# Kernel tuning notes

Hardware: AMD Instinct MI355X
Metric: run time of the kernel (lower is better)

Reference implementation:

```python
import jax, jax.numpy as jnp
import numpy as np

D_MODEL = 1024
D_STATE = 16
EXPAND = 2
D_CONV = 4
D_INNER = EXPAND * D_MODEL          # 2048
DT_RANK = D_MODEL // 16             # 64
B = 2
L = 1024
EPS = 1e-5


def setup_inputs() -> dict:
    key = jax.random.key(0)
    ks = jax.random.split(key, 8)
    s = 0.02
    return {
        "x": jax.random.normal(ks[0], (B, L, D_MODEL), jnp.float32),
        "ln_gamma": jnp.ones((D_MODEL,), jnp.float32),
        "ln_beta": jnp.zeros((D_MODEL,), jnp.float32),
        "in_proj_w": jax.random.normal(ks[1], (2 * D_INNER, D_MODEL), jnp.float32) * s,
        "conv_w": jax.random.normal(ks[2], (D_INNER, 1, D_CONV), jnp.float32) * s,
        "conv_b": jnp.zeros((D_INNER,), jnp.float32),
        "x_proj_w": jax.random.normal(ks[3], (DT_RANK + 2 * D_STATE, D_INNER), jnp.float32) * s,
        "dt_proj_w": jax.random.normal(ks[4], (D_INNER, DT_RANK), jnp.float32) * s,
        "dt_proj_b": jax.random.normal(ks[5], (D_INNER,), jnp.float32) * 0.01,
        "A_log": jnp.log(jnp.tile(jnp.arange(1, D_STATE + 1, dtype=jnp.float32), (D_INNER, 1))),
        "D_skip": jnp.ones((D_INNER,), jnp.float32),
        "out_proj_w": jax.random.normal(ks[6], (D_MODEL, D_INNER), jnp.float32) * s,
    }


def _layernorm(x, g, b):
    mu = jnp.mean(x, axis=-1, keepdims=True)
    var = jnp.mean((x - mu) ** 2, axis=-1, keepdims=True)
    return (x - mu) * jax.lax.rsqrt(var + EPS) * g + b


def _mamba_forward(x, ln_gamma, ln_beta, in_proj_w, conv_w, conv_b,
                   x_proj_w, dt_proj_w, dt_proj_b, A_log, D_skip, out_proj_w):
    residual = x
    xn = _layernorm(x, ln_gamma, ln_beta)

    # in_proj -> split into ssm input u and gate z   (b, l, 2*d_inner)
    xz = jnp.einsum('bld,ed->ble', xn, in_proj_w)
    u, z = jnp.split(xz, 2, axis=-1)

    # causal depthwise conv1d (padding = d_conv-1 on the left, truncated to L)
    uc = jnp.transpose(u, (0, 2, 1))  # (b, d_inner, l)
    uc = jax.lax.conv_general_dilated(
        uc, conv_w, window_strides=(1,), padding=[(D_CONV - 1, 0)],
        feature_group_count=D_INNER,
        dimension_numbers=('NCH', 'OIH', 'NCH'))
    uc = uc + conv_b[None, :, None]
    u = jax.nn.silu(jnp.transpose(uc, (0, 2, 1)))  # (b, l, d_inner)

    # selective SSM
    A = -jnp.exp(A_log)                              # (d_inner, d_state)
    x_dbl = jnp.einsum('bld,ed->ble', u, x_proj_w)   # (b, l, dt_rank+2*n)
    dt, Bm, Cm = jnp.split(x_dbl, [DT_RANK, DT_RANK + D_STATE], axis=-1)
    delta = jax.nn.softplus(jnp.einsum('blr,dr->bld', dt, dt_proj_w) + dt_proj_b)

    def step(h, inputs):
        d_t, B_t, C_t, u_t = inputs            # (b,di) (b,n) (b,n) (b,di)
        dA = jnp.exp(d_t[..., None] * A)       # (b, di, n)
        h = dA * h + (d_t * u_t)[..., None] * B_t[:, None, :]
        y = jnp.einsum('bdn,bn->bd', h, C_t)
        return h, y

    h0 = jnp.zeros((x.shape[0], D_INNER, D_STATE), x.dtype)
    xs = (jnp.moveaxis(delta, 1, 0), jnp.moveaxis(Bm, 1, 0),
          jnp.moveaxis(Cm, 1, 0), jnp.moveaxis(u, 1, 0))
    _, ys = jax.lax.scan(step, h0, xs)
    y = jnp.moveaxis(ys, 0, 1) + u * D_skip     # (b, l, d_inner)

    y = y * jax.nn.silu(z)                      # gated output
    out = jnp.einsum('ble,de->bld', y, out_proj_w)
    # dropout is identity in eval mode
    return out + residual


def reference(x, ln_gamma, ln_beta, in_proj_w, conv_w, conv_b,
              x_proj_w, dt_proj_w, dt_proj_b, A_log, D_skip, out_proj_w):
    return _mamba_forward(x, ln_gamma, ln_beta, in_proj_w, conv_w, conv_b,
                          x_proj_w, dt_proj_w, dt_proj_b, A_log, D_skip, out_proj_w)
```

## Files before the change

### kernel.cpp

```cpp
#include <hip/hip_runtime.h>

#define D_MODEL 1024
#define D_STATE 16
#define D_INNER 2048
#define DT_RANK 64
#define NBATCH 2
#define SEQ_L 1024
#define M_ROWS (NBATCH * SEQ_L)
#define CHUNK 32
#define NCHUNK (SEQ_L / CHUNK)

typedef __bf16 bf16x8 __attribute__((ext_vector_type(8)));
typedef float f32x4 __attribute__((ext_vector_type(4)));
typedef unsigned short u16;
typedef unsigned int u32;
typedef u16 u16x4 __attribute__((ext_vector_type(4)));
typedef u16 u16x8 __attribute__((ext_vector_type(8)));

__device__ __forceinline__ float bf2f(u16 h) {
    return __uint_as_float(((unsigned)h) << 16);
}
__device__ __forceinline__ u16 f2bf(float f) {
    unsigned u = __float_as_uint(f);
    u += 0x7fff + ((u >> 16) & 1);
    return (u16)(u >> 16);
}

__global__ __launch_bounds__(256) void prep(
    const float* __restrict__ s0, const float* __restrict__ s1,
    const float* __restrict__ s2, const float* __restrict__ s3,
    u16* __restrict__ d0, u16* __restrict__ d1,
    u16* __restrict__ d2, u16* __restrict__ d3,
    const float* __restrict__ x, const float* __restrict__ g,
    const float* __restrict__ b, u16* __restrict__ xn,
    float* __restrict__ xd) {
    int blk = blockIdx.x;
    if (blk < 6464) {
        int idx = blk * 256 + threadIdx.x;
        const float4* s; u16* dp; int i;
        if (idx < 1048576)      { s = (const float4*)s0; i = idx;           dp = d0; }
        else if (idx < 1572864) { s = (const float4*)s1; i = idx - 1048576; dp = d1; }
        else if (idx < 1622016) { s = (const float4*)s2; i = idx - 1572864; dp = d2; }
        else                    { s = (const float4*)s3; i = idx - 1622016; dp = d3; }
        float4 v = s[i];
        u16x4 o = {f2bf(v.x), f2bf(v.y), f2bf(v.z), f2bf(v.w)};
        *(u16x4*)(dp + (size_t)i * 4) = o;
        return;
    }
    if (blk < 6656) {
        int zi = (blk - 6464) * 256 + threadIdx.x;
        ((float4*)xd)[zi] = (float4){0.f, 0.f, 0.f, 0.f};
        return;
    }
    int row = blk - 6656;
    const float4* xr = (const float4*)(x + (size_t)row * D_MODEL);
    float4 v = xr[threadIdx.x];
    float s  = v.x + v.y + v.z + v.w;
    float ss = v.x * v.x + v.y * v.y + v.z * v.z + v.w * v.w;
#pragma unroll
    for (int off = 32; off > 0; off >>= 1) {
        s  += __shfl_down(s,  off, 64);
        ss += __shfl_down(ss, off, 64);
    }
    __shared__ float sh_s[4], sh_ss[4];
    int wid = threadIdx.x >> 6;
    if ((threadIdx.x & 63) == 0) { sh_s[wid] = s; sh_ss[wid] = ss; }
    __syncthreads();
    float mu  = (sh_s[0] + sh_s[1] + sh_s[2] + sh_s[3]) * (1.0f / D_MODEL);
    float var = (sh_ss[0] + sh_ss[1] + sh_ss[2] + sh_ss[3]) * (1.0f / D_MODEL) - mu * mu;
    float rs = rsqrtf(var + 1e-5f);
    int c0 = threadIdx.x * 4;
    float vv[4] = {v.x, v.y, v.z, v.w};
#pragma unroll
    for (int j = 0; j < 4; j++) {
        int c = c0 + j;
        float o = (vv[j] - mu) * rs * g[c] + b[c];
        xn[(size_t)row * D_MODEL + c] = f2bf(o);
    }
}

template <int BM, int BN, int WM, int WN, int MODE>
__global__ __launch_bounds__(256) void gemm_lds(
    const __bf16* __restrict__ A, const __bf16* __restrict__ W,
    int K, int Ksteps, int ldC,
    float* __restrict__ outF, u16* __restrict__ outB) {
    constexpr int WCOLS = BN / (WN * 16);
    __shared__ __bf16 As[BM * 32];
    __shared__ __bf16 Bs[BN * 32];
    int tid  = threadIdx.x;
    int lane = tid & 63;
    int wid  = tid >> 6;
    int l16  = lane & 15;
    int quad = lane >> 4;
    int wr = wid / WCOLS;
    int wc = wid % WCOLS;
    int m0 = blockIdx.y * BM;
    int n0 = blockIdx.x * BN;
    int kbase = blockIdx.z * Ksteps * 32;

    f32x4 acc[WM][WN];
#pragma unroll
    for (int mi = 0; mi < WM; mi++)
#pragma unroll
        for (int nj = 0; nj < WN; nj++)
            acc[mi][nj] = (f32x4){0.f, 0.f, 0.f, 0.f};

    for (int ki = 0; ki < Ksteps; ki++) {
        int k0 = kbase + ki * 32;
        __syncthreads();
#pragma unroll
        for (int i = 0; i < BM / 64; i++) {
            int t   = i * 256 + tid;
            int row = t >> 2;
            int cg  = (t & 3) ^ ((row >> 1) & 3);
            __builtin_amdgcn_global_load_lds(
                (const __attribute__((address_space(1))) u32*)(A + (size_t)(m0 + row) * K + k0 + cg * 8),
                (__attribute__((address_space(3))) u32*)(As + (i * 256 + wid * 64) * 8),
                16, 0, 0);
        }
#pragma unroll
        for (int i = 0; i < BN / 64; i++) {
            int t   = i * 256 + tid;
            int row = t >> 2;
            int cg  = (t & 3) ^ ((row >> 1) & 3);
            __builtin_amdgcn_global_load_lds(
                (const __attribute__((address_space(1))) u32*)(W + (size_t)(n0 + row) * K + k0 + cg * 8),
                (__attribute__((address_space(3))) u32*)(Bs + (i * 256 + wid * 64) * 8),
                16, 0, 0);
        }
        __syncthreads();

        bf16x8 af[WM], bfr[WN];
#pragma unroll
        for (int mi = 0; mi < WM; mi++) {
            int r  = wr * WM * 16 + mi * 16 + l16;
            int cg = quad ^ ((r >> 1) & 3);
            af[mi] = *(const bf16x8*)(As + r * 32 + cg * 8);
        }
#pragma unroll
        for (int nj = 0; nj < WN; nj++) {
            int r  = wc * WN * 16 + nj * 16 + l16;
            int cg = quad ^ ((r >> 1) & 3);
            bfr[nj] = *(const bf16x8*)(Bs + r * 32 + cg * 8);
        }
#pragma unroll
        for (int mi = 0; mi < WM; mi++)
#pragma unroll
            for (int nj = 0; nj < WN; nj++)
                acc[mi][nj] = __builtin_amdgcn_mfma_f32_16x16x32_bf16(
                    af[mi], bfr[nj], acc[mi][nj], 0, 0, 0);
    }

    float* outP = (MODE == 4) ? outF + (size_t)blockIdx.z * M_ROWS * ldC : outF;
#pragma unroll
    for (int mi = 0; mi < WM; mi++) {
#pragma unroll
        for (int nj = 0; nj < WN; nj++) {
            int col = n0 + wc * WN * 16 + nj * 16 + l16;
#pragma unroll
            for (int r = 0; r < 4; r++) {
                int row = m0 + wr * WM * 16 + mi * 16 + quad * 4 + r;
                float v = acc[mi][nj][r];
                if (MODE == 0) {
                    outB[(size_t)row * ldC + col] = f2bf(v);
                } else {
                    outP[(size_t)row * ldC + col] = v;
                }
            }
        }
    }
}

__global__ __launch_bounds__(256) void out_reduce(
    const float* __restrict__ p, const float* __restrict__ x,
    float* __restrict__ out) {
    int idx = blockIdx.x * 256 + threadIdx.x;
    const int N = M_ROWS * D_MODEL;
    float4 a = ((const float4*)p)[idx];
    float4 b = ((const float4*)(p + N))[idx];
    float4 c = ((const float4*)(p + 2 * N))[idx];
    float4 d = ((const float4*)(p + 3 * N))[idx];
    float4 r = ((const float4*)x)[idx];
    float4 o;
    o.x = a.x + b.x + c.x + d.x + r.x;
    o.y = a.y + b.y + c.y + d.y + r.y;
    o.z = a.z + b.z + c.z + d.z + r.z;
    o.w = a.w + b.w + c.w + d.w + r.w;
    ((float4*)out)[idx] = o;
}

__global__ __launch_bounds__(256) void gemm_xp(
    const __bf16* __restrict__ A, const __bf16* __restrict__ W,
    float* __restrict__ outF) {
    const int K = D_INNER, Ksplit = D_INNER / 8, Nw = 96;
    int lane = threadIdx.x & 63;
    int wid  = threadIdx.x >> 6;
    int m0 = blockIdx.y * 64;
    int n0 = blockIdx.x * 64;
    int kc = blockIdx.z;
    int l16  = lane & 15;
    int quad = lane >> 4;
    int mrow = m0 + wid * 16 + l16;

    const __bf16* ap = A + (size_t)mrow * K + kc * Ksplit + quad * 8;
    const __bf16* wp[4];
#pragma unroll
    for (int j = 0; j < 4; j++) {
        int nc = n0 + j * 16 + l16;
        if (nc > Nw - 1) nc = Nw - 1;
        wp[j] = W + (size_t)nc * K + kc * Ksplit + quad * 8;
    }
    f32x4 acc[4];
#pragma unroll
    for (int j = 0; j < 4; j++) acc[j] = (f32x4){0.f, 0.f, 0.f, 0.f};

    for (int k = 0; k < Ksplit; k += 32) {
        bf16x8 a = *(const bf16x8*)ap;
        ap += 32;
#pragma unroll
        for (int j = 0; j < 4; j++) {
            bf16x8 bfr = *(const bf16x8*)wp[j];
            wp[j] += 32;
            acc[j] = __builtin_amdgcn_mfma_f32_16x16x32_bf16(a, bfr, acc[j], 0, 0, 0);
        }
    }
#pragma unroll
    for (int j = 0; j < 4; j++) {
        int col = n0 + j * 16 + l16;
        if (col < Nw) {
#pragma unroll
            for (int r = 0; r < 4; r++) {
                int row = m0 + wid * 16 + quad * 4 + r;
                atomicAdd(outF + (size_t)row * 96 + col, acc[j][r]);
            }
        }
    }
}

__global__ __launch_bounds__(256) void gemm_dt(
    const float* __restrict__ A, const __bf16* __restrict__ W,
    const float* __restrict__ bias, u16* __restrict__ outB16) {
    int lane = threadIdx.x & 63;
    int wid  = threadIdx.x >> 6;
    int m0 = blockIdx.y * 64;
    int n0 = blockIdx.x * 64;
    int l16  = lane & 15;
    int quad = lane >> 4;
    int mrow = m0 + wid * 16 + l16;

    const float* ap = A + (size_t)mrow * 96 + quad * 8;
    const __bf16* wp[4];
#pragma unroll
    for (int j = 0; j < 4; j++) {
        int nc = n0 + j * 16 + l16;
        wp[j] = W + (size_t)nc * DT_RANK + quad * 8;
    }
    f32x4 acc[4];
#pragma unroll
    for (int j = 0; j < 4; j++) acc[j] = (f32x4){0.f, 0.f, 0.f, 0.f};

#pragma unroll
    for (int k = 0; k < DT_RANK; k += 32) {
        float4 v0 = *(const float4*)(ap);
        float4 v1 = *(const float4*)(ap + 4);
        ap += 32;
        u16x8 pk;
        pk[0] = f2bf(v0.x); pk[1] = f2bf(v0.y); pk[2] = f2bf(v0.z); pk[3] = f2bf(v0.w);
        pk[4] = f2bf(v1.x); pk[5] = f2bf(v1.y); pk[6] = f2bf(v1.z); pk[7] = f2bf(v1.w);
        bf16x8 a = __builtin_bit_cast(bf16x8, pk);
#pragma unroll
        for (int j = 0; j < 4; j++) {
            bf16x8 bfr = *(const bf16x8*)wp[j];
            wp[j] += 32;
            acc[j] = __builtin_amdgcn_mfma_f32_16x16x32_bf16(a, bfr, acc[j], 0, 0, 0);
        }
    }
#pragma unroll
    for (int j = 0; j < 4; j++) {
        int col = n0 + j * 16 + l16;
#pragma unroll
        for (int r = 0; r < 4; r++) {
            int row = m0 + wid * 16 + quad * 4 + r;
            float t = acc[j][r] + bias[col];
            float sp = (t > 20.f) ? t : log1pf(__expf(t));
            outB16[(size_t)row * D_INNER + col] = f2bf(sp);
        }
    }
}

__global__ __launch_bounds__(256) void conv_silu(
    const u16* __restrict__ xz, const float* __restrict__ cw,
    const float* __restrict__ cb, u16* __restrict__ uc) {
    int idx = blockIdx.x * 256 + threadIdx.x;
    int base = idx * 8;
    int d = base & (D_INNER - 1);
    int m = base >> 11;
    int t = m & (SEQ_L - 1);
    float s[8];
    {
        float4 b0 = *(const float4*)(cb + d);
        float4 b1 = *(const float4*)(cb + d + 4);
        s[0] = b0.x; s[1] = b0.y; s[2] = b0.z; s[3] = b0.w;
        s[4] = b1.x; s[5] = b1.y; s[6] = b1.z; s[7] = b1.w;
    }
#pragma unroll
    for (int j = 0; j < 4; j++) {
        int tt = t - 3 + j;
        if (tt >= 0) {
            u16x8 uv = *(const u16x8*)(xz + (size_t)(m - 3 + j) * (2 * D_INNER) + d);
#pragma unroll
            for (int q = 0; q < 8; q++) {
                s[q] += cw[(d + q) * 4 + j] * bf2f(uv[q]);
            }
        }
    }
    u16x8 o;
#pragma unroll
    for (int q = 0; q < 8; q++) {
        float sig = 1.f / (1.f + __expf(-s[q]));
        o[q] = f2bf(s[q] * sig);
    }
    *(u16x8*)(uc + base) = o;
}

__global__ __launch_bounds__(256) void scan_chunk(
    const u16* __restrict__ delta, const u16* __restrict__ uc,
    const float* __restrict__ xd, const float* __restrict__ A_log,
    float* __restrict__ Pst, float* __restrict__ Sst) {
    __shared__ float Bsh[CHUNK][16];
    int tid  = threadIdx.x;
    int lane = tid & 63;
    int w    = tid >> 6;
    int dsub = lane & 15;
    int g    = lane >> 4;
    int n0   = g * 4;
    int c = blockIdx.x, b = blockIdx.z;
    int d = blockIdx.y * 64 + w * 16 + dsub;
    int mbase = b * SEQ_L + c * CHUNK;

    if (tid < CHUNK * 4) {
        int row = tid >> 2, q = tid & 3;
        *(float4*)&Bsh[row][q * 4] =
            *(const float4*)(xd + (size_t)(mbase + row) * 96 + DT_RANK + q * 4);
    }
    __syncthreads();

    float a[4];
    {
        float4 a0 = *(const float4*)(A_log + d * D_STATE + n0);
        a[0] = -__expf(a0.x); a[1] = -__expf(a0.y);
        a[2] = -__expf(a0.z); a[3] = -__expf(a0.w);
    }
    float P[4] = {1.f, 1.f, 1.f, 1.f}, S[4] = {0.f, 0.f, 0.f, 0.f};

    for (int t0 = 0; t0 < CHUNK; t0 += 4) {
        float dlv[4], uv[4];
#pragma unroll
        for (int i = 0; i < 4; i++) {
            int m = mbase + t0 + i;
            dlv[i] = bf2f(delta[(size_t)m * D_INNER + d]);
            uv[i]  = bf2f(uc[(size_t)m * D_INNER + d]);
        }
#pragma unroll
        for (int i = 0; i < 4; i++) {
            float c1 = dlv[i] * uv[i];
#pragma unroll
            for (int j = 0; j < 4; j++) {
                float dA = __expf(dlv[i] * a[j]);
                P[j] *= dA;
                S[j] = dA * S[j] + c1 * Bsh[t0 + i][n0 + j];
            }
        }
    }
    size_t s = ((size_t)(b * D_INNER + d) * NCHUNK + c) * D_STATE + n0;
    *(float4*)(Pst + s) = (float4){P[0], P[1], P[2], P[3]};
    *(float4*)(Sst + s) = (float4){S[0], S[1], S[2], S[3]};
}

__global__ __launch_bounds__(256) void scan_combine(
    const float* __restrict__ Pst, const float* __restrict__ Sst,
    float* __restrict__ Hin) {
    int idx = blockIdx.x * 256 + threadIdx.x;
    int bd = idx >> 4;
    int n  = idx & 15;
    float h = 0.f;
#pragma unroll
    for (int c = 0; c < NCHUNK; ++c) {
        size_t s = ((size_t)bd * NCHUNK + c) * D_STATE + n;
        Hin[s] = h;
        h = Pst[s] * h + Sst[s];
    }
}

__global__ __launch_bounds__(256) void scan_apply(
    const u16* __restrict__ delta, const u16* __restrict__ uc,
    const float* __restrict__ xd, const u16* __restrict__ xz,
    const float* __restrict__ A_log, const float* __restrict__ Dsk,
    const float* __restrict__ Hin, u16* __restrict__ yg) {
    __shared__ float BCs[CHUNK][32];
    int tid  = threadIdx.x;
    int lane = tid & 63;
    int w    = tid >> 6;
    int dsub = lane & 15;
    int g    = lane >> 4;
    int n0   = g * 4;
    int c = blockIdx.x, b = blockIdx.z;
    int d = blockIdx.y * 64 + w * 16 + dsub;
    int mbase = b * SEQ_L + c * CHUNK;

    {
        int row = tid >> 3, q = tid & 7;
        *(float4*)&BCs[row][q * 4] =
            *(const float4*)(xd + (size_t)(mbase + row) * 96 + DT_RANK + q * 4);
    }
    __syncthreads();

    float a[4];
    {
        float4 a0 = *(const float4*)(A_log + d * D_STATE + n0);
        a[0] = -__expf(a0.x); a[1] = -__expf(a0.y);
        a[2] = -__expf(a0.z); a[3] = -__expf(a0.w);
    }
    float h[4];
    {
        float4 h0 = *(const float4*)(Hin +
            (((size_t)(b * D_INNER + d) * NCHUNK + c) * D_STATE + n0));
        h[0] = h0.x; h[1] = h0.y; h[2] = h0.z; h[3] = h0.w;
    }
    float dsk = Dsk[d];

    for (int t0 = 0; t0 < CHUNK; t0 += 4) {
        float dlv[4], uv[4], zv[4];
#pragma unroll
        for (int i = 0; i < 4; i++) {
            int m = mbase + t0 + i;
            dlv[i] = bf2f(delta[(size_t)m * D_INNER + d]);
            uv[i]  = bf2f(uc[(size_t)m * D_INNER + d]);
            zv[i]  = bf2f(xz[(size_t)m * (2 * D_INNER) + D_INNER + d]);
        }
#pragma unroll
        for (int i = 0; i < 4; i++) {
            int t = t0 + i;
            float c1 = dlv[i] * uv[i];
            float y = 0.f;
#pragma unroll
            for (int j = 0; j < 4; j++) {
                float dA = __expf(dlv[i] * a[j]);
                h[j] = dA * h[j] + c1 * BCs[t][n0 + j];
                y += h[j] * BCs[t][16 + n0 + j];
            }
            y += __shfl_xor(y, 16);
            y += __shfl_xor(y, 32);
            if (g == 0) {
                float z = zv[i];
                float yv = y + uv[i] * dsk;
                float gt = z / (1.f + __expf(-z));
                yg[(size_t)(mbase + t) * D_INNER + d] = f2bf(yv * gt);
            }
        }
    }
}

extern "C" void kernel_launch(void* const* d_in, const int* in_sizes, int n_in,
                              void* d_out, int out_size, void* d_ws, size_t ws_size,
                              hipStream_t stream) {
    const float* x         = (const float*)d_in[0];
    const float* ln_g      = (const float*)d_in[1];
    const float* ln_b      = (const float*)d_in[2];
    const float* in_proj_w = (const float*)d_in[3];
    const float* conv_w    = (const float*)d_in[4];
    const float* conv_b    = (const float*)d_in[5];
    const float* x_proj_w  = (const float*)d_in[6];
    const float* dt_proj_w = (const float*)d_in[7];
    const float* dt_proj_b = (const float*)d_in[8];
    const float* A_log     = (const float*)d_in[9];
    const float* Dsk       = (const float*)d_in[10];
    const float* out_proj_w= (const float*)d_in[11];

    char* ws = (char*)d_ws;
    u16* xn   = (u16*)ws;    ws += (size_t)M_ROWS * D_MODEL * 2;
    u16* xz   = (u16*)ws;    ws += (size_t)M_ROWS * 2 * D_INNER * 2;
    u16* ucv  = (u16*)ws;    ws += (size_t)M_ROWS * D_INNER * 2;
    float* xd = (float*)ws;  ws += (size_t)M_ROWS * 96 * 4;
    u16* dl   = (u16*)ws;    ws += (size_t)M_ROWS * D_INNER * 2;
    u16* yg   = (u16*)ws;    ws += (size_t)M_ROWS * D_INNER * 2;
    u16* w_in = (u16*)ws;    ws += (size_t)4194304 * 2;
    u16* w_out= (u16*)ws;    ws += (size_t)2097152 * 2;
    u16* w_xp = (u16*)ws;    ws += (size_t)196608 * 2;
    u16* w_dt = (u16*)ws;    ws += (size_t)131072 * 2;
    float* Pst = (float*)ws; ws += (size_t)NBATCH * D_INNER * D_STATE * NCHUNK * 4;
    float* Sst = (float*)ws; ws += (size_t)NBATCH * D_INNER * D_STATE * NCHUNK * 4;
    float* Hin = (float*)ws; ws += (size_t)NBATCH * D_INNER * D_STATE * NCHUNK * 4;
    float* opart = (float*)ws;

    prep<<<6656 + M_ROWS, 256, 0, stream>>>(
        in_proj_w, out_proj_w, x_proj_w, dt_proj_w, w_in, w_out, w_xp, w_dt,
        x, ln_g, ln_b, xn, xd);
    gemm_lds<64, 128, 4, 2, 0><<<dim3(4096 / 128, M_ROWS / 64, 1), 256, 0, stream>>>(
        (const __bf16*)xn, (const __bf16*)w_in, D_MODEL, D_MODEL / 32, 2 * D_INNER,
        nullptr, xz);
    conv_silu<<<(M_ROWS * D_INNER) / (256 * 8), 256, 0, stream>>>(xz, conv_w, conv_b, ucv);
    gemm_xp<<<dim3(2, 32, 8), 256, 0, stream>>>(
        (const __bf16*)ucv, (const __bf16*)w_xp, xd);
    gemm_dt<<<dim3(32, 32, 1), 256, 0, stream>>>(
        xd, (const __bf16*)w_dt, dt_proj_b, dl);
    dim3 sgrid(NCHUNK, D_INNER / 64, NBATCH);
    scan_chunk<<<sgrid, 256, 0, stream>>>(dl, ucv, xd, A_log, Pst, Sst);
    scan_combine<<<(NBATCH * D_INNER * D_STATE) / 256, 256, 0, stream>>>(Pst, Sst, Hin);
    scan_apply<<<sgrid, 256, 0, stream>>>(dl, ucv, xd, xz, A_log, Dsk, Hin, yg);
    gemm_lds<64, 128, 4, 2, 4><<<dim3(1024 / 128, M_ROWS / 64, 4), 256, 0, stream>>>(
        (const __bf16*)yg, (const __bf16*)w_out, D_INNER, D_INNER / 4 / 32, D_MODEL,
        opart, nullptr);
    out_reduce<<<(M_ROWS * D_MODEL / 4) / 256, 256, 0, stream>>>(
        opart, x, (float*)d_out);
}
```

Measured before the change: 273.3 us.

## Use atomic split-K output accumulation, seed residual in prep, scalarize conversions

The out-projection split-K GEMM now atomically adds its partial sums straight into the output buffer. The prep kernel first seeds that buffer with the residual x, so the separate reduce kernel and the partial-sum buffer are gone. The weight-conversion path in prep and the conv_silu kernel are also changed from vectorized float4 and 8-wide accesses to one element per thread, which launches four and eight times as many blocks. The atomic path removes a kernel launch and a round trip through the partial buffers, but it adds atomic contention and makes the sum order nondeterministic, while the de-vectorized loads and stores are likely less efficient.

Result: no change. 277.9 us (+1.7%).

```diff
diff --git a/kernel.cpp b/kernel.cpp
--- a/kernel.cpp
+++ b/kernel.cpp
@@ -14,7 +14,6 @@
 typedef float f32x4 __attribute__((ext_vector_type(4)));
 typedef unsigned short u16;
 typedef unsigned int u32;
-typedef u16 u16x4 __attribute__((ext_vector_type(4)));
 typedef u16 u16x8 __attribute__((ext_vector_type(8)));
 
 __device__ __forceinline__ float bf2f(u16 h) {
@@ -33,26 +32,32 @@
     u16* __restrict__ d2, u16* __restrict__ d3,
     const float* __restrict__ x, const float* __restrict__ g,
     const float* __restrict__ b, u16* __restrict__ xn,
-    float* __restrict__ xd) {
+    float* __restrict__ xd, float* __restrict__ outSeed) {
     int blk = blockIdx.x;
-    if (blk < 6464) {
+    if (blk < 25856) {
         int idx = blk * 256 + threadIdx.x;
-        const float4* s; u16* dp; int i;
-        if (idx < 1048576)      { s = (const float4*)s0; i = idx;           dp = d0; }
-        else if (idx < 1572864) { s = (const float4*)s1; i = idx - 1048576; dp = d1; }
-        else if (idx < 1622016) { s = (const float4*)s2; i = idx - 1572864; dp = d2; }
-        else                    { s = (const float4*)s3; i = idx - 1622016; dp = d3; }
-        float4 v = s[i];
-        u16x4 o = {f2bf(v.x), f2bf(v.y), f2bf(v.z), f2bf(v.w)};
-        *(u16x4*)(dp + (size_t)i * 4) = o;
+        if (idx < 4194304) {
+            d0[idx] = f2bf(s0[idx]);
+        } else if (idx < 6291456) {
+            int i = idx - 4194304; d1[i] = f2bf(s1[i]);
+        } else if (idx < 6488064) {
+            int i = idx - 6291456; d2[i] = f2bf(s2[i]);
+        } else {
+            int i = idx - 6488064; d3[i] = f2bf(s3[i]);
+        }
         return;
     }
-    if (blk < 6656) {
-        int zi = (blk - 6464) * 256 + threadIdx.x;
+    if (blk < 26048) {
+        int zi = (blk - 25856) * 256 + threadIdx.x;
         ((float4*)xd)[zi] = (float4){0.f, 0.f, 0.f, 0.f};
         return;
     }
-    int row = blk - 6656;
+    if (blk < 28096) {
+        int si = (blk - 26048) * 256 + threadIdx.x;
+        ((float4*)outSeed)[si] = ((const float4*)x)[si];
+        return;
+    }
+    int row = blk - 28096;
     const float4* xr = (const float4*)(x + (size_t)row * D_MODEL);
     float4 v = xr[threadIdx.x];
     float s  = v.x + v.y + v.z + v.w;
@@ -151,7 +156,6 @@
                     af[mi], bfr[nj], acc[mi][nj], 0, 0, 0);
     }
 
-    float* outP = (MODE == 4) ? outF + (size_t)blockIdx.z * M_ROWS * ldC : outF;
 #pragma unroll
     for (int mi = 0; mi < WM; mi++) {
 #pragma unroll
@@ -164,29 +168,11 @@
                 if (MODE == 0) {
                     outB[(size_t)row * ldC + col] = f2bf(v);
                 } else {
-                    outP[(size_t)row * ldC + col] = v;
+                    atomicAdd(outF + (size_t)row * ldC + col, v);
                 }
             }
         }
     }
-}
-
-__global__ __launch_bounds__(256) void out_reduce(
-    const float* __restrict__ p, const float* __restrict__ x,
-    float* __restrict__ out) {
-    int idx = blockIdx.x * 256 + threadIdx.x;
-    const int N = M_ROWS * D_MODEL;
-    float4 a = ((const float4*)p)[idx];
-    float4 b = ((const float4*)(p + N))[idx];
-    float4 c = ((const float4*)(p + 2 * N))[idx];
-    float4 d = ((const float4*)(p + 3 * N))[idx];
-    float4 r = ((const float4*)x)[idx];
-    float4 o;
-    o.x = a.x + b.x + c.x + d.x + r.x;
-    o.y = a.y + b.y + c.y + d.y + r.y;
-    o.z = a.z + b.z + c.z + d.z + r.z;
-    o.w = a.w + b.w + c.w + d.w + r.w;
-    ((float4*)out)[idx] = o;
 }
 
 __global__ __launch_bounds__(256) void gemm_xp(
@@ -292,35 +278,20 @@
     const u16* __restrict__ xz, const float* __restrict__ cw,
     const float* __restrict__ cb, u16* __restrict__ uc) {
     int idx = blockIdx.x * 256 + threadIdx.x;
-    int base = idx * 8;
-    int d = base & (D_INNER - 1);
-    int m = base >> 11;
+    int d = idx & (D_INNER - 1);
+    int m = idx >> 11;
     int t = m & (SEQ_L - 1);
-    float s[8];
-    {
-        float4 b0 = *(const float4*)(cb + d);
-        float4 b1 = *(const float4*)(cb + d + 4);
-        s[0] = b0.x; s[1] = b0.y; s[2] = b0.z; s[3] = b0.w;
-        s[4] = b1.x; s[5] = b1.y; s[6] = b1.z; s[7] = b1.w;
-    }
+    float s = cb[d];
 #pragma unroll
     for (int j = 0; j < 4; j++) {
         int tt = t - 3 + j;
         if (tt >= 0) {
-            u16x8 uv = *(const u16x8*)(xz + (size_t)(m - 3 + j) * (2 * D_INNER) + d);
-#pragma unroll
-            for (int q = 0; q < 8; q++) {
-                s[q] += cw[(d + q) * 4 + j] * bf2f(uv[q]);
-            }
-        }
-    }
-    u16x8 o;
-#pragma unroll
-    for (int q = 0; q < 8; q++) {
-        float sig = 1.f / (1.f + __expf(-s[q]));
-        o[q] = f2bf(s[q] * sig);
-    }
-    *(u16x8*)(uc + base) = o;
+            s += cw[d * 4 + j] *
+                 bf2f(xz[(size_t)(m - 3 + j) * (2 * D_INNER) + d]);
+        }
+    }
+    float sig = 1.f / (1.f + __expf(-s));
+    uc[idx] = f2bf(s * sig);
 }
 
 __global__ __launch_bounds__(256) void scan_chunk(
@@ -490,16 +461,17 @@
     u16* w_dt = (u16*)ws;    ws += (size_t)131072 * 2;
     float* Pst = (float*)ws; ws += (size_t)NBATCH * D_INNER * D_STATE * NCHUNK * 4;
     float* Sst = (float*)ws; ws += (size_t)NBATCH * D_INNER * D_STATE * NCHUNK * 4;
-    float* Hin = (float*)ws; ws += (size_t)NBATCH * D_INNER * D_STATE * NCHUNK * 4;
-    float* opart = (float*)ws;
-
-    prep<<<6656 + M_ROWS, 256, 0, stream>>>(
+    float* Hin = (float*)ws;
+
+    float* out = (float*)d_out;
+
+    prep<<<28096 + M_ROWS, 256, 0, stream>>>(
         in_proj_w, out_proj_w, x_proj_w, dt_proj_w, w_in, w_out, w_xp, w_dt,
-        x, ln_g, ln_b, xn, xd);
+        x, ln_g, ln_b, xn, xd, out);
     gemm_lds<64, 128, 4, 2, 0><<<dim3(4096 / 128, M_ROWS / 64, 1), 256, 0, stream>>>(
         (const __bf16*)xn, (const __bf16*)w_in, D_MODEL, D_MODEL / 32, 2 * D_INNER,
         nullptr, xz);
-    conv_silu<<<(M_ROWS * D_INNER) / (256 * 8), 256, 0, stream>>>(xz, conv_w, conv_b, ucv);
+    conv_silu<<<(M_ROWS * D_INNER) / 256, 256, 0, stream>>>(xz, conv_w, conv_b, ucv);
     gemm_xp<<<dim3(2, 32, 8), 256, 0, stream>>>(
         (const __bf16*)ucv, (const __bf16*)w_xp, xd);
     gemm_dt<<<dim3(32, 32, 1), 256, 0, stream>>>(
@@ -508,9 +480,7 @@
     scan_chunk<<<sgrid, 256, 0, stream>>>(dl, ucv, xd, A_log, Pst, Sst);
     scan_combine<<<(NBATCH * D_INNER * D_STATE) / 256, 256, 0, stream>>>(Pst, Sst, Hin);
     scan_apply<<<sgrid, 256, 0, stream>>>(dl, ucv, xd, xz, A_log, Dsk, Hin, yg);
-    gemm_lds<64, 128, 4, 2, 4><<<dim3(1024 / 128, M_ROWS / 64, 4), 256, 0, stream>>>(
+    gemm_lds<64, 128, 4, 2, 5><<<dim3(1024 / 128, M_ROWS / 64, 4), 256, 0, stream>>>(
         (const __bf16*)yg, (const __bf16*)w_out, D_INNER, D_INNER / 4 / 32, D_MODEL,
-        opart, nullptr);
-    out_reduce<<<(M_ROWS * D_MODEL / 4) / 256, 256, 0, stream>>>(
-        opart, x, (float*)d_out);
-}
+        out, nullptr);
+}
```
